# Performance work log

Measured on AMD Instinct MI355X. Metric: run time of the kernel, lower is better.

Reference implementation:

```python
import jax, jax.numpy as jnp
import numpy as np

B, M, V, D = 2048, 2, 25, 64      # batch, max_body, joints, input channels
C1, C2, K, U = 128, 256, 3, 256   # gcn hidden, gcn out, A kernel size, lstm units
NJ, NB = M * V * U, M * U         # joint / body state widths
SD = NJ + NB + U                  # full state dim = 13568


def _hs(z):
    # keras hard_sigmoid
    return jnp.clip(0.2 * z + 0.5, 0.0, 1.0)


def _lstm_step(z, c):
    i = _hs(z[..., :U])
    f = _hs(z[..., U:2 * U])
    g = jnp.tanh(z[..., 2 * U:3 * U])
    o = _hs(z[..., 3 * U:])
    c2 = f * c + i * g
    return o * jnp.tanh(c2), c2


def _forget_bias(shape_prefix):
    z = jnp.zeros(shape_prefix + (U,), jnp.float32)
    return jnp.concatenate([z, jnp.ones_like(z), z, z], axis=-1)


def setup_inputs() -> dict:
    key = jax.random.key(0)
    ks = jax.random.split(key, 16)
    f = lambda i, shape, s: jax.random.normal(ks[i], shape, jnp.float32) * s
    x = f(0, (B, M * V * D), 1.0)
    h0 = f(1, (B, SD), 0.1)
    c0 = f(2, (B, SD), 0.1)
    A = jax.random.uniform(ks[3], (K, V, V), jnp.float32)
    A = A / jnp.sum(A, axis=-1, keepdims=True)  # row-normalized adjacency stack
    edge_importance = jnp.ones((2, K, V, V), jnp.float32)
    return dict(
        x=x, h0=h0, c0=c0, A=A, edge_importance=edge_importance,
        wg0=f(4, (D, C1 * K), 0.05), bg0=jnp.zeros((C1 * K,), jnp.float32),
        wg1=f(5, (C1, C2 * K), 0.05), bg1=jnp.zeros((C2 * K,), jnp.float32),
        wr1=f(6, (C1, C2), 0.05), br1=jnp.zeros((C2,), jnp.float32),
        kernel=f(7, (C2, 4 * U), 0.02),
        kernel_body=f(8, (V * C2, 4 * U), 0.01),
        kernel_whole=f(9, (M * V * C2, 4 * U), 0.005),
        rk=f(10, (U, 4 * U), 0.02),
        rk_body=f(11, (U, 4 * U), 0.02),
        rk_whole=f(12, (U, 4 * U), 0.02),
        bias=_forget_bias((M, V)),
        bias_body=_forget_bias((M,)),
        bias_whole=_forget_bias((1,)),
    )


def reference(x, h0, c0, A, edge_importance, wg0, bg0, wg1, bg1, wr1, br1,
              kernel, kernel_body, kernel_whole, rk, rk_body, rk_whole,
              bias, bias_body, bias_whole):
    N = B * M
    xg = x.reshape(N, V, D)
    # --- GCN layer 0: 1x1 conv -> split K -> edge-weighted adjacency einsum ---
    y = (xg @ wg0 + bg0).reshape(N, V, K, C1)
    y = jnp.einsum('nvkc,kvw->nwc', y, edge_importance[0] * A)
    y = jax.nn.relu(y)
    # --- GCN layer 1 (channels change -> residual 1x1 conv) ---
    res = y @ wr1 + br1
    z = (y @ wg1 + bg1).reshape(N, V, K, C2)
    z = jnp.einsum('nvkc,kvw->nwc', z, edge_importance[1] * A) + res
    feat = jax.nn.relu(z).reshape(B, M, V, C2)
    # --- unpack multi-scale state ---
    h_j = h0[:, :NJ].reshape(B, M, V, U)
    c_j = c0[:, :NJ].reshape(B, M, V, U)
    h_b = h0[:, NJ:NJ + NB].reshape(B, M, U)
    c_b = c0[:, NJ:NJ + NB].reshape(B, M, U)
    h_w = h0[:, NJ + NB:]
    c_w = c0[:, NJ + NB:]
    # --- joint-scale gates ---
    zj = jnp.einsum('bmvc,cu->bmvu', feat, kernel) + h_j @ rk + bias
    h_j2, c_j2 = _lstm_step(zj, c_j)
    # --- body-scale gates ---
    zb = feat.reshape(B, M, V * C2) @ kernel_body + h_b @ rk_body + bias_body
    h_b2, c_b2 = _lstm_step(zb, c_b)
    # --- whole-scale gates ---
    zw = feat.reshape(B, M * V * C2) @ kernel_whole + h_w @ rk_whole + bias_whole[0]
    h_w2, c_w2 = _lstm_step(zw, c_w)
    h_new = jnp.concatenate([h_j2.reshape(B, NJ), h_b2.reshape(B, NB), h_w2], axis=-1)
    return h_new
```

## Files before the change

### kernel.cpp

```cpp
#include <hip/hip_runtime.h>
#include <hip/hip_bf16.h>
#include <math.h>

constexpr int Bn = 2048, Mm = 2, Vv = 25, Dd = 64;
constexpr int C1 = 128, C2 = 256, Kk = 3, Uu = 256;
constexpr int NJ = Mm*Vv*Uu;
constexpr int NBd = Mm*Uu;
constexpr int SD = NJ+NBd+Uu;
constexpr int Nn = Bn*Mm;
constexpr int N3 = Nn*Vv;
constexpr int NCH = 2;
constexpr int NnC = Nn/NCH;
constexpr int RCn = NnC*Vv;

typedef __bf16 v8bf __attribute__((ext_vector_type(8)));
typedef float f32x16 __attribute__((ext_vector_type(16)));

__device__ __forceinline__ float hsig(float z){ return fminf(fmaxf(0.2f*z+0.5f,0.f),1.f); }
__device__ __forceinline__ float ftanh(float x){
  float e = __expf(2.f*x);
  return 1.f - 2.f*__frcp_rn(e+1.f);
}
__device__ __forceinline__ unsigned short f2bs(float x){
  __hip_bfloat16 h = __float2bfloat16(x);
  unsigned short s; __builtin_memcpy(&s, &h, 2); return s;
}
__device__ __forceinline__ float bs2f(unsigned short s){
  unsigned u = ((unsigned)s)<<16; float f; __builtin_memcpy(&f,&u,4); return f;
}

#if defined(__has_builtin)
#if __has_builtin(__builtin_amdgcn_global_load_lds)
#define HAS_ALD 1
#endif
#endif
#ifndef HAS_ALD
#define HAS_ALD 0
#endif
__device__ __forceinline__ void stage16(unsigned short* dst_base, int lane, const void* src){
#if HAS_ALD
  __builtin_amdgcn_global_load_lds(
      (const __attribute__((address_space(1))) unsigned int*)src,
      (__attribute__((address_space(3))) unsigned int*)dst_base, 16, 0, 0);
#else
  *(uint4*)(dst_base + lane*8) = *(const uint4*)src;
#endif
}

template<int SW, typename TI>
__global__ __launch_bounds__(SW*3) void kMix(
    const TI* __restrict__ src, const float* __restrict__ Amat,
    const float* __restrict__ ei, int eoff, unsigned short* __restrict__ dst)
{
  __shared__ float xs[Vv*SW];
  __shared__ float as[Kk*Vv*Vv];
  const int n = blockIdx.x, t = threadIdx.x;
  const TI* srow = src + (size_t)n*(Vv*SW);
  for(int i=t;i<Vv*SW;i+=SW*3){
    if constexpr (sizeof(TI)==2) xs[i]=bs2f((unsigned short)srow[i]);
    else xs[i]=srow[i];
  }
  for(int i=t;i<Kk*Vv*Vv;i+=SW*3) as[i]=ei[eoff+i]*Amat[i];
  __syncthreads();
  const int k = t/SW, d = t%SW;
  float acc[Vv];
  #pragma unroll
  for(int w=0;w<Vv;++w) acc[w]=0.f;
  for(int v=0;v<Vv;++v){
    float xv = xs[v*SW+d];
    const float* ap = &as[k*625 + v*25];
    #pragma unroll
    for(int w=0;w<Vv;++w) acc[w] += ap[w]*xv;
  }
  unsigned short* drow = dst + (size_t)n*(Vv*3*SW);
  for(int w=0;w<Vv;++w) drow[w*(3*SW) + t] = f2bs(acc[w]);
}

template<int MODE>
__device__ __forceinline__ size_t hoffOf(int row){
  if constexpr (MODE==0){ int b=row/50, j=row-b*50; return (size_t)b*SD + j*256; }
  else if constexpr (MODE==1){ int b=row>>1, m=row&1; return (size_t)b*SD + NJ + m*256; }
  else return (size_t)row*SD + NJ + NBd;
}

template<int MODE>
__global__ __launch_bounds__(256) void kConvW(
    const float* __restrict__ Wm, const float* __restrict__ Wr,
    unsigned short* __restrict__ out, int total)
{
  int i = blockIdx.x*256 + threadIdx.x;
  if(i>=total) return;
  int e = i&7, ln = (i>>3)&63, l31 = ln&31, l5 = ln>>5;
  float v;
  if constexpr (MODE<=2){
    constexpr int KF = (MODE==0)?256:(MODE==1)?6400:12800;
    constexpr int NKT = (KF+256)/32;
    int fb = (i>>9)&15, kt = (i>>13)%NKT, ublk = i/(NKT*8192);
    int kh = fb&1, cg = fb>>1;
    int k = kt*32 + l5*8 + kh*16 + e;
    int g = cg&3, uu = (cg>>2)*32 + l31;
    int col = g*256 + ublk*64 + uu;
    v = (k<KF) ? Wm[(size_t)k*1024+col] : Wr[(size_t)(k-KF)*1024+col];
  } else if constexpr (MODE==3){
    int fb = (i>>9)&15, kt = i>>13;
    int kh = fb&1, cg = fb>>1;
    int k = kt*32 + l5*8 + kh*16 + e;
    int col = cg*32 + l31;
    v = (k<384) ? Wm[(size_t)(k&127)*768 + (k>>7)*256 + col]
                : Wr[(size_t)(k-384)*256 + col];
  } else {
    int fb = (i>>9)&7, kt = i>>12;
    int kh = fb&1, cg = fb>>1;
    int k = kt*32 + l5*8 + kh*16 + e;
    int col = cg*32 + l31;
    v = Wm[(size_t)(k&63)*384 + (k>>6)*128 + col];
  }
  out[i] = f2bs(v);
}

template<int MODE>
__global__ __launch_bounds__(256) void kConvH(
    const float* __restrict__ h0, unsigned short* __restrict__ dst, int total4)
{
  int i = blockIdx.x*256 + threadIdx.x;
  if(i>=total4) return;
  int row = i>>6, k4 = (i&63)*4;
  const float* s = h0 + hoffOf<MODE>(row) + k4;
  float4 f = *(const float4*)s;
  uint2 o;
  o.x = (unsigned)f2bs(f.x) | ((unsigned)f2bs(f.y)<<16);
  o.y = (unsigned)f2bs(f.z) | ((unsigned)f2bs(f.w)<<16);
  *(uint2*)(dst + (size_t)i*4) = o;
}

template<int MODE, int MR>
__global__ __launch_bounds__(256,2) void kLSTMm(
    const unsigned short* __restrict__ featb, const unsigned short* __restrict__ h0b,
    const float* __restrict__ c0, const unsigned short* __restrict__ Wcat,
    const float* __restrict__ bias, float* __restrict__ outp, int KC)
{
  constexpr int KF = (MODE==0)?256:(MODE==1)?6400:12800;
  constexpr int KT = KF+256;
  constexpr int NKT = KT/32;
  constexpr int ROWS = (MODE==0)?N3:(MODE==1)?Nn:Bn;
  constexpr int NRG = MR/64;
  constexpr int NAF = (MR/32)*2;
  __shared__ unsigned short Afr[2][NAF*512];
  __shared__ unsigned short Bfr[2][16*512];
  const int t = threadIdx.x;
  const int bx = blockIdx.x;
  const int r0 = (bx>>2)*MR;
  const int ublk = bx&3;
  const int z = (MODE==0)?0:blockIdx.y;
  const int kBeg = z*KC, kEnd = min(KT, kBeg+KC);
  const int lane = t&63, wid = t>>6;
  const int wr = wid>>1, w2 = wid&1;
  const int l31 = lane&31, l5 = lane>>5;

  f32x16 acc[NRG][4];
  #pragma unroll
  for(int rg=0;rg<NRG;++rg)
    #pragma unroll
    for(int g=0;g<4;++g)
      #pragma unroll
      for(int j=0;j<16;++j) acc[rg][g][j]=0.f;

  auto stageA = [&](unsigned short* dstb, int k0){
    #pragma unroll
    for(int i=0;i<NRG;++i){
      int fi = i*256 + t;
      int row = r0 + (fi>>7)*32 + l31;
      int kc = (lane>>5) + ((fi>>6)&1)*2;
      int kg = k0 + kc*8;
      const unsigned short* src = (kg < KF)
          ? featb + (size_t)row*KF + kg
          : h0b   + (size_t)row*256 + (kg - KF);
      stage16(dstb + (size_t)(i*256 + wid*64)*8, lane, src);
    }
  };
  auto stageB = [&](unsigned short* dstb, int k0){
    const unsigned short* wt = Wcat + ((size_t)ublk*NKT + (k0>>5))*8192;
    #pragma unroll
    for(int i=0;i<4;++i){
      int fi = i*256 + t;
      stage16(dstb + (size_t)(i*256 + wid*64)*8, lane, wt + (size_t)fi*8);
    }
  };

  stageA(Afr[0], kBeg); stageB(Bfr[0], kBeg);
  __syncthreads();
  const int nst = (kEnd-kBeg)>>5;
  for(int s=0; s<nst; ++s){
    const int cur = s&1;
    if(s+1<nst){ stageA(Afr[cur^1], kBeg+(s+1)*32); stageB(Bfr[cur^1], kBeg+(s+1)*32); }
    #pragma unroll
    for(int kh=0; kh<2; ++kh){
      v8bf a[NRG];
      #pragma unroll
      for(int rg=0;rg<NRG;++rg)
        a[rg] = *(const v8bf*)&Afr[cur][((wr*NRG+rg)*2+kh)*512 + lane*8];
      #pragma unroll
      for(int g=0; g<4; ++g){
        v8bf b = *(const v8bf*)&Bfr[cur][((w2*4+g)*2+kh)*512 + lane*8];
        #pragma unroll
        for(int rg=0;rg<NRG;++rg)
          acc[rg][g] = __builtin_amdgcn_mfma_f32_32x32x16_bf16(a[rg], b, acc[rg][g], 0, 0, 0);
      }
    }
    __syncthreads();
  }

  const int u = ublk*64 + w2*32 + l31;
  if constexpr (MODE==0){
    #pragma unroll
    for(int rg=0;rg<NRG;++rg){
      #pragma unroll
      for(int reg=0; reg<16; ++reg){
        int row = r0 + (wr*NRG+rg)*32 + (reg&3) + 8*(reg>>2) + 4*l5;
        int b = row/50, j = row - b*50;
        size_t hoff = (size_t)b*SD + j*256;
        int boff = j*1024;
        float zi = acc[rg][0][reg] + bias[boff + u];
        float zf = acc[rg][1][reg] + bias[boff + 256 + u];
        float zg = acc[rg][2][reg] + bias[boff + 512 + u];
        float zo = acc[rg][3][reg] + bias[boff + 768 + u];
        float iv=hsig(zi), fv=hsig(zf), gv=ftanh(zg), ov=hsig(zo);
        float cc = c0[hoff+u];
        float c2 = fv*cc + iv*gv;
        outp[hoff+u] = ov*ftanh(c2);
      }
    }
  } else {
    #pragma unroll
    for(int rg=0;rg<NRG;++rg){
      #pragma unroll
      for(int reg=0; reg<16; ++reg){
        int row = r0 + (wr*NRG+rg)*32 + (reg&3) + 8*(reg>>2) + 4*l5;
        float* base = outp + ((size_t)z*ROWS + row)*1024 + u;
        base[0]   = acc[rg][0][reg];
        base[256] = acc[rg][1][reg];
        base[512] = acc[rg][2][reg];
        base[768] = acc[rg][3][reg];
      }
    }
  }
}

__global__ __launch_bounds__(256,2) void kGC2(
    const unsigned short* __restrict__ ycat, const unsigned short* __restrict__ yb,
    const unsigned short* __restrict__ Wc2, const float* __restrict__ bg1,
    const float* __restrict__ br1, const float* __restrict__ Amat,
    const float* __restrict__ ei, unsigned short* __restrict__ featb)
{
  __shared__ unsigned short Afr[2][4*512];
  __shared__ unsigned short Bfr[2][16*512];
  __shared__ float asums[75];
  const int t = threadIdx.x;
  const int r0 = blockIdx.x*64;
  if(t<75){
    int k=t/25, w=t%25; float s=0.f;
    for(int v=0;v<25;++v) s += ei[1875 + k*625+v*25+w]*Amat[k*625+v*25+w];
    asums[t]=s;
  }
  const int lane = t&63, wid = t>>6;
  const int wr = wid>>1, w2 = wid&1;
  const int l31 = lane&31, l5 = lane>>5;
  f32x16 acc[4];
  #pragma unroll
  for(int g=0;g<4;++g)
    #pragma unroll
    for(int j=0;j<16;++j) acc[g][j]=0.f;

  auto stageA = [&](unsigned short* dst, int k0){
    int fi = t;
    int row = r0 + (fi>>7)*32 + l31;
    int kc = (lane>>5) + ((fi>>6)&1)*2;
    int kg = k0 + kc*8;
    const unsigned short* src = (kg<384) ? ycat + (size_t)row*384 + kg
                                         : yb   + (size_t)row*128 + (kg-384);
    stage16(dst + (size_t)(wid*64)*8, lane, src);
  };
  auto stageB = [&](unsigned short* dst, int k0){
    const unsigned short* wt = Wc2 + (size_t)(k0>>5)*8192;
    #pragma unroll
    for(int i=0;i<4;++i){
      int fi = i*256 + t;
      stage16(dst + (size_t)(i*256 + wid*64)*8, lane, wt + (size_t)fi*8);
    }
  };

  stageA(Afr[0],0); stageB(Bfr[0],0);
  __syncthreads();
  for(int s=0; s<16; ++s){
    const int cur = s&1;
    if(s+1<16){ stageA(Afr[cur^1],(s+1)*32); stageB(Bfr[cur^1],(s+1)*32); }
    #pragma unroll
    for(int kh=0; kh<2; ++kh){
      v8bf a = *(const v8bf*)&Afr[cur][(wr*2+kh)*512 + lane*8];
      #pragma unroll
      for(int g=0; g<4; ++g){
        v8bf b = *(const v8bf*)&Bfr[cur][((w2*4+g)*2+kh)*512 + lane*8];
        acc[g] = __builtin_amdgcn_mfma_f32_32x32x16_bf16(a, b, acc[g], 0, 0, 0);
      }
    }
    __syncthreads();
  }
  #pragma unroll
  for(int reg=0; reg<16; ++reg){
    int row = r0 + wr*32 + (reg&3) + 8*(reg>>2) + 4*l5;
    int w = row % 25;
    float a0w = asums[w], a1w = asums[25+w], a2w = asums[50+w];
    #pragma unroll
    for(int g=0; g<4; ++g){
      int cc = w2*128 + g*32 + l31;
      float b = br1[cc] + a0w*bg1[cc] + a1w*bg1[256+cc] + a2w*bg1[512+cc];
      featb[(size_t)row*256 + cc] = f2bs(fmaxf(acc[g][reg] + b, 0.f));
    }
  }
}

__global__ __launch_bounds__(256,2) void kGC1(
    const unsigned short* __restrict__ xcat, const unsigned short* __restrict__ Wc1,
    const float* __restrict__ bg0, const float* __restrict__ Amat,
    const float* __restrict__ ei, unsigned short* __restrict__ yb)
{
  __shared__ unsigned short Afr[2][4*512];
  __shared__ unsigned short Bfr[2][8*512];
  __shared__ float asums[75];
  const int t = threadIdx.x;
  const int r0 = blockIdx.x*64;
  if(t<75){
    int k=t/25, w=t%25; float s=0.f;
    for(int v=0;v<25;++v) s += ei[k*625+v*25+w]*Amat[k*625+v*25+w];
    asums[t]=s;
  }
  const int lane = t&63, wid = t>>6;
  const int wr = wid>>1, w2 = wid&1;
  const int l31 = lane&31, l5 = lane>>5;
  f32x16 acc[2];
  #pragma unroll
  for(int g=0;g<2;++g)
    #pragma unroll
    for(int j=0;j<16;++j) acc[g][j]=0.f;

  auto stageA = [&](unsigned short* dst, int k0){
    int fi = t;
    int row = r0 + (fi>>7)*32 + l31;
    int kc = (lane>>5) + ((fi>>6)&1)*2;
    int kg = k0 + kc*8;
    stage16(dst + (size_t)(wid*64)*8, lane, xcat + (size_t)row*192 + kg);
  };
  auto stageB = [&](unsigned short* dst, int k0){
    const unsigned short* wt = Wc1 + (size_t)(k0>>5)*4096;
    #pragma unroll
    for(int i=0;i<2;++i){
      int fi = i*256 + t;
      stage16(dst + (size_t)(i*256 + wid*64)*8, lane, wt + (size_t)fi*8);
    }
  };

  stageA(Afr[0],0); stageB(Bfr[0],0);
  __syncthreads();
  for(int s=0; s<6; ++s){
    const int cur = s&1;
    if(s+1<6){ stageA(Afr[cur^1],(s+1)*32); stageB(Bfr[cur^1],(s+1)*32); }
    #pragma unroll
    for(int kh=0; kh<2; ++kh){
      v8bf a = *(const v8bf*)&Afr[cur][(wr*2+kh)*512 + lane*8];
      #pragma unroll
      for(int g=0; g<2; ++g){
        v8bf b = *(const v8bf*)&Bfr[cur][((w2*2+g)*2+kh)*512 + lane*8];
        acc[g] = __builtin_amdgcn_mfma_f32_32x32x16_bf16(a, b, acc[g], 0, 0, 0);
      }
    }
    __syncthreads();
  }
  #pragma unroll
  for(int reg=0; reg<16; ++reg){
    int row = r0 + wr*32 + (reg&3) + 8*(reg>>2) + 4*l5;
    int w = row % 25;
    float a0w = asums[w], a1w = asums[25+w], a2w = asums[50+w];
    #pragma unroll
    for(int g=0; g<2; ++g){
      int cc = w2*64 + g*32 + l31;
      float b = a0w*bg0[cc] + a1w*bg0[128+cc] + a2w*bg0[256+cc];
      yb[(size_t)row*128 + cc] = f2bs(fmaxf(acc[g][reg] + b, 0.f));
    }
  }
}

template<int MODE>
__global__ __launch_bounds__(256) void kFin(
    const float* __restrict__ part, const float* __restrict__ c0,
    const float* __restrict__ bias, float* __restrict__ out, int S)
{
  constexpr int ROWS = (MODE==1)?Nn:Bn;
  const int row = blockIdx.x, u = threadIdx.x;
  size_t hoff = hoffOf<MODE>(row);
  int boff = (MODE==1)?((row&1)*1024):0;
  float zg4[4] = { bias[boff+u], bias[boff+256+u], bias[boff+512+u], bias[boff+768+u] };
  for(int s=0;s<S;++s){
    const float* p = part + ((size_t)s*ROWS + row)*1024;
    #pragma unroll
    for(int g=0;g<4;++g) zg4[g] += p[g*256+u];
  }
  float iv=hsig(zg4[0]), fv=hsig(zg4[1]), gv=ftanh(zg4[2]), ov=hsig(zg4[3]);
  float cc = c0[hoff+u];
  float c2 = fv*cc + iv*gv;
  out[hoff+u] = ov*ftanh(c2);
}

extern "C" void kernel_launch(void* const* d_in, const int* in_sizes, int n_in,
                              void* d_out, int out_size, void* d_ws, size_t ws_size,
                              hipStream_t stream)
{
  const float* x   = (const float*)d_in[0];
  const float* h0  = (const float*)d_in[1];
  const float* c0  = (const float*)d_in[2];
  const float* A   = (const float*)d_in[3];
  const float* ei  = (const float*)d_in[4];
  const float* wg0 = (const float*)d_in[5];
  const float* bg0 = (const float*)d_in[6];
  const float* wg1 = (const float*)d_in[7];
  const float* bg1 = (const float*)d_in[8];
  const float* wr1 = (const float*)d_in[9];
  const float* br1 = (const float*)d_in[10];
  const float* kern  = (const float*)d_in[11];
  const float* kernB = (const float*)d_in[12];
  const float* kernW = (const float*)d_in[13];
  const float* rk    = (const float*)d_in[14];
  const float* rkB   = (const float*)d_in[15];
  const float* rkW   = (const float*)d_in[16];
  const float* bias  = (const float*)d_in[17];
  const float* biasB = (const float*)d_in[18];
  const float* biasW = (const float*)d_in[19];
  float* out = (float*)d_out;
  char* wsb  = (char*)d_ws;

  unsigned short* featb = (unsigned short*)wsb;
  unsigned short* WbJ = (unsigned short*)(wsb + 52428800);
  unsigned short* WbB = WbJ + 524288;
  unsigned short* WbW = WbB + 6815744;
  unsigned short* Wc2 = WbW + 13369344;
  unsigned short* Wc1 = Wc2 + 131072;
  char* dyn = wsb + 94158848;
  unsigned short* ycat = (unsigned short*)dyn;
  unsigned short* xcat = ycat;
  unsigned short* yb   = (unsigned short*)(dyn + 39321600);
  unsigned short* h0bJ = (unsigned short*)dyn;
  float* part = (float*)dyn;
  unsigned short* hB = (unsigned short*)(wsb + 146587648);
  unsigned short* hW = hB + 1048576;

  kConvW<0><<<(524288+255)/256,   256, 0, stream>>>(kern,  rk,  WbJ, 524288);
  kConvW<1><<<(6815744+255)/256,  256, 0, stream>>>(kernB, rkB, WbB, 6815744);
  kConvW<2><<<(13369344+255)/256, 256, 0, stream>>>(kernW, rkW, WbW, 13369344);
  kConvW<3><<<(131072+255)/256,   256, 0, stream>>>(wg1, wr1, Wc2, 131072);
  kConvW<4><<<(24576+255)/256,    256, 0, stream>>>(wg0, nullptr, Wc1, 24576);
  kConvH<1><<<(262144+255)/256, 256, 0, stream>>>(h0, hB, 262144);
  kConvH<2><<<(131072+255)/256, 256, 0, stream>>>(h0, hW, 131072);

  for(int c=0;c<NCH;++c){
    const float* xc = x + (size_t)c*NnC*(Vv*Dd);
    kMix<64,float>          <<<NnC, 192, 0, stream>>>(xc, A, ei, 0, xcat);
    kGC1<<<RCn/64, 256, 0, stream>>>(xcat, Wc1, bg0, A, ei, yb);
    kMix<128,unsigned short><<<NnC, 384, 0, stream>>>(yb, A, ei, 1875, ycat);
    kGC2<<<RCn/64, 256, 0, stream>>>(ycat, yb, Wc2, bg1, br1, A, ei,
                                     featb + (size_t)c*RCn*256);
  }
  kConvH<0><<<(6553600+255)/256, 256, 0, stream>>>(h0, h0bJ, 6553600);
  kLSTMm<0,64><<<(N3/64)*4, 256, 0, stream>>>(featb, h0bJ, c0, WbJ, bias, out, 512);
  kLSTMm<1,128><<<dim3((Nn/128)*4,3), 256, 0, stream>>>(featb, hB, nullptr, WbB, nullptr, part, 2240);
  kFin<1><<<Nn, 256, 0, stream>>>(part, c0, biasB, out, 3);
  kLSTMm<2,128><<<dim3((Bn/128)*4,6), 256, 0, stream>>>(featb, hW, nullptr, WbW, nullptr, part, 2176);
  kFin<2><<<Bn, 256, 0, stream>>>(part, c0, biasW, out, 6);
}
```

Baseline: 746.3 us.

## Load GEMM B fragments directly into registers and shrink LSTM row tiles

```diff
diff --git a/kernel.cpp b/kernel.cpp
--- a/kernel.cpp
+++ b/kernel.cpp
@@ -133,7 +133,7 @@
   *(uint2*)(dst + (size_t)i*4) = o;
 }
 
-template<int MODE, int MR>
+template<int MODE>
 __global__ __launch_bounds__(256,2) void kLSTMm(
     const unsigned short* __restrict__ featb, const unsigned short* __restrict__ h0b,
     const float* __restrict__ c0, const unsigned short* __restrict__ Wcat,
@@ -143,13 +143,10 @@
   constexpr int KT = KF+256;
   constexpr int NKT = KT/32;
   constexpr int ROWS = (MODE==0)?N3:(MODE==1)?Nn:Bn;
-  constexpr int NRG = MR/64;
-  constexpr int NAF = (MR/32)*2;
-  __shared__ unsigned short Afr[2][NAF*512];
-  __shared__ unsigned short Bfr[2][16*512];
+  __shared__ unsigned short Afr[2][4*512];
   const int t = threadIdx.x;
   const int bx = blockIdx.x;
-  const int r0 = (bx>>2)*MR;
+  const int r0 = (bx>>2)*64;
   const int ublk = bx&3;
   const int z = (MODE==0)?0:blockIdx.y;
   const int kBeg = z*KC, kEnd = min(KT, kBeg+KC);
@@ -157,91 +154,78 @@
   const int wr = wid>>1, w2 = wid&1;
   const int l31 = lane&31, l5 = lane>>5;
 
-  f32x16 acc[NRG][4];
-  #pragma unroll
-  for(int rg=0;rg<NRG;++rg)
-    #pragma unroll
-    for(int g=0;g<4;++g)
-      #pragma unroll
-      for(int j=0;j<16;++j) acc[rg][g][j]=0.f;
+  f32x16 acc[4];
+  #pragma unroll
+  for(int g=0;g<4;++g)
+    #pragma unroll
+    for(int j=0;j<16;++j) acc[g][j]=0.f;
 
   auto stageA = [&](unsigned short* dstb, int k0){
-    #pragma unroll
-    for(int i=0;i<NRG;++i){
-      int fi = i*256 + t;
-      int row = r0 + (fi>>7)*32 + l31;
-      int kc = (lane>>5) + ((fi>>6)&1)*2;
-      int kg = k0 + kc*8;
-      const unsigned short* src = (kg < KF)
-          ? featb + (size_t)row*KF + kg
-          : h0b   + (size_t)row*256 + (kg - KF);
-      stage16(dstb + (size_t)(i*256 + wid*64)*8, lane, src);
-    }
-  };
-  auto stageB = [&](unsigned short* dstb, int k0){
-    const unsigned short* wt = Wcat + ((size_t)ublk*NKT + (k0>>5))*8192;
-    #pragma unroll
-    for(int i=0;i<4;++i){
-      int fi = i*256 + t;
-      stage16(dstb + (size_t)(i*256 + wid*64)*8, lane, wt + (size_t)fi*8);
-    }
-  };
-
-  stageA(Afr[0], kBeg); stageB(Bfr[0], kBeg);
+    int row = r0 + wr*32 + l31;
+    int kg = k0 + (w2*2 + l5)*8;
+    const unsigned short* src = (kg < KF)
+        ? featb + (size_t)row*KF + kg
+        : h0b   + (size_t)row*256 + (kg - KF);
+    stage16(dstb + (size_t)(wid*64)*8, lane, src);
+  };
+  auto loadB = [&](v8bf (&b)[8], int k0){
+    const unsigned short* wt = Wcat + ((size_t)ublk*NKT + (k0>>5))*8192 + (size_t)lane*8;
+    #pragma unroll
+    for(int g=0; g<4; ++g)
+      #pragma unroll
+      for(int kh=0; kh<2; ++kh)
+        b[g*2+kh] = *(const v8bf*)(wt + ((w2*4+g)*2+kh)*512);
+  };
+  auto mstep = [&](const v8bf (&b)[8], const unsigned short* Ab){
+    #pragma unroll
+    for(int kh=0; kh<2; ++kh){
+      v8bf a = *(const v8bf*)&Ab[(wr*2+kh)*512 + lane*8];
+      #pragma unroll
+      for(int g=0; g<4; ++g)
+        acc[g] = __builtin_amdgcn_mfma_f32_32x32x16_bf16(a, b[g*2+kh], acc[g], 0, 0, 0);
+    }
+  };
+
+  v8bf bA[8], bB[8];
+  stageA(Afr[0], kBeg); loadB(bA, kBeg);
   __syncthreads();
   const int nst = (kEnd-kBeg)>>5;
-  for(int s=0; s<nst; ++s){
-    const int cur = s&1;
-    if(s+1<nst){ stageA(Afr[cur^1], kBeg+(s+1)*32); stageB(Bfr[cur^1], kBeg+(s+1)*32); }
-    #pragma unroll
-    for(int kh=0; kh<2; ++kh){
-      v8bf a[NRG];
-      #pragma unroll
-      for(int rg=0;rg<NRG;++rg)
-        a[rg] = *(const v8bf*)&Afr[cur][((wr*NRG+rg)*2+kh)*512 + lane*8];
-      #pragma unroll
-      for(int g=0; g<4; ++g){
-        v8bf b = *(const v8bf*)&Bfr[cur][((w2*4+g)*2+kh)*512 + lane*8];
-        #pragma unroll
-        for(int rg=0;rg<NRG;++rg)
-          acc[rg][g] = __builtin_amdgcn_mfma_f32_32x32x16_bf16(a[rg], b, acc[rg][g], 0, 0, 0);
-      }
-    }
+  for(int s=0; s<nst; s+=2){
+    int k0 = kBeg + s*32;
+    stageA(Afr[1], k0+32); loadB(bB, k0+32);
+    mstep(bA, Afr[0]);
+    __syncthreads();
+    if(s+2<nst){ stageA(Afr[0], k0+64); loadB(bA, k0+64); }
+    mstep(bB, Afr[1]);
     __syncthreads();
   }
 
   const int u = ublk*64 + w2*32 + l31;
   if constexpr (MODE==0){
     #pragma unroll
-    for(int rg=0;rg<NRG;++rg){
-      #pragma unroll
-      for(int reg=0; reg<16; ++reg){
-        int row = r0 + (wr*NRG+rg)*32 + (reg&3) + 8*(reg>>2) + 4*l5;
-        int b = row/50, j = row - b*50;
-        size_t hoff = (size_t)b*SD + j*256;
-        int boff = j*1024;
-        float zi = acc[rg][0][reg] + bias[boff + u];
-        float zf = acc[rg][1][reg] + bias[boff + 256 + u];
-        float zg = acc[rg][2][reg] + bias[boff + 512 + u];
-        float zo = acc[rg][3][reg] + bias[boff + 768 + u];
-        float iv=hsig(zi), fv=hsig(zf), gv=ftanh(zg), ov=hsig(zo);
-        float cc = c0[hoff+u];
-        float c2 = fv*cc + iv*gv;
-        outp[hoff+u] = ov*ftanh(c2);
-      }
+    for(int reg=0; reg<16; ++reg){
+      int row = r0 + wr*32 + (reg&3) + 8*(reg>>2) + 4*l5;
+      int b = row/50, j = row - b*50;
+      size_t hoff = (size_t)b*SD + j*256;
+      int boff = j*1024;
+      float zi = acc[0][reg] + bias[boff + u];
+      float zf = acc[1][reg] + bias[boff + 256 + u];
+      float zg = acc[2][reg] + bias[boff + 512 + u];
+      float zo = acc[3][reg] + bias[boff + 768 + u];
+      float iv=hsig(zi), fv=hsig(zf), gv=ftanh(zg), ov=hsig(zo);
+      float cc = c0[hoff+u];
+      float c2 = fv*cc + iv*gv;
+      outp[hoff+u] = ov*ftanh(c2);
     }
   } else {
     #pragma unroll
-    for(int rg=0;rg<NRG;++rg){
-      #pragma unroll
-      for(int reg=0; reg<16; ++reg){
-        int row = r0 + (wr*NRG+rg)*32 + (reg&3) + 8*(reg>>2) + 4*l5;
-        float* base = outp + ((size_t)z*ROWS + row)*1024 + u;
-        base[0]   = acc[rg][0][reg];
-        base[256] = acc[rg][1][reg];
-        base[512] = acc[rg][2][reg];
-        base[768] = acc[rg][3][reg];
-      }
+    for(int reg=0; reg<16; ++reg){
+      int row = r0 + wr*32 + (reg&3) + 8*(reg>>2) + 4*l5;
+      float* base = outp + ((size_t)z*ROWS + row)*1024 + u;
+      base[0]   = acc[0][reg];
+      base[256] = acc[1][reg];
+      base[512] = acc[2][reg];
+      base[768] = acc[3][reg];
     }
   }
 }
@@ -253,7 +237,6 @@
     const float* __restrict__ ei, unsigned short* __restrict__ featb)
 {
   __shared__ unsigned short Afr[2][4*512];
-  __shared__ unsigned short Bfr[2][16*512];
   __shared__ float asums[75];
   const int t = threadIdx.x;
   const int r0 = blockIdx.x*64;
@@ -272,37 +255,39 @@
     for(int j=0;j<16;++j) acc[g][j]=0.f;
 
   auto stageA = [&](unsigned short* dst, int k0){
-    int fi = t;
-    int row = r0 + (fi>>7)*32 + l31;
-    int kc = (lane>>5) + ((fi>>6)&1)*2;
-    int kg = k0 + kc*8;
+    int row = r0 + wr*32 + l31;
+    int kg = k0 + (w2*2 + l5)*8;
     const unsigned short* src = (kg<384) ? ycat + (size_t)row*384 + kg
                                          : yb   + (size_t)row*128 + (kg-384);
     stage16(dst + (size_t)(wid*64)*8, lane, src);
   };
-  auto stageB = [&](unsigned short* dst, int k0){
-    const unsigned short* wt = Wc2 + (size_t)(k0>>5)*8192;
-    #pragma unroll
-    for(int i=0;i<4;++i){
-      int fi = i*256 + t;
-      stage16(dst + (size_t)(i*256 + wid*64)*8, lane, wt + (size_t)fi*8);
-    }
-  };
-
-  stageA(Afr[0],0); stageB(Bfr[0],0);
+  auto loadB = [&](v8bf (&b)[8], int k0){
+    const unsigned short* wt = Wc2 + (size_t)(k0>>5)*8192 + (size_t)lane*8;
+    #pragma unroll
+    for(int g=0; g<4; ++g)
+      #pragma unroll
+      for(int kh=0; kh<2; ++kh)
+        b[g*2+kh] = *(const v8bf*)(wt + ((w2*4+g)*2+kh)*512);
+  };
+  auto mstep = [&](const v8bf (&b)[8], const unsigned short* Ab){
+    #pragma unroll
+    for(int kh=0; kh<2; ++kh){
+      v8bf a = *(const v8bf*)&Ab[(wr*2+kh)*512 + lane*8];
+      #pragma unroll
+      for(int g=0; g<4; ++g)
+        acc[g] = __builtin_amdgcn_mfma_f32_32x32x16_bf16(a, b[g*2+kh], acc[g], 0, 0, 0);
+    }
+  };
+
+  v8bf bA[8], bB[8];
+  stageA(Afr[0],0); loadB(bA,0);
   __syncthreads();
-  for(int s=0; s<16; ++s){
-    const int cur = s&1;
-    if(s+1<16){ stageA(Afr[cur^1],(s+1)*32); stageB(Bfr[cur^1],(s+1)*32); }
-    #pragma unroll
-    for(int kh=0; kh<2; ++kh){
-      v8bf a = *(const v8bf*)&Afr[cur][(wr*2+kh)*512 + lane*8];
-      #pragma unroll
-      for(int g=0; g<4; ++g){
-        v8bf b = *(const v8bf*)&Bfr[cur][((w2*4+g)*2+kh)*512 + lane*8];
-        acc[g] = __builtin_amdgcn_mfma_f32_32x32x16_bf16(a, b, acc[g], 0, 0, 0);
-      }
-    }
+  for(int s=0; s<16; s+=2){
+    stageA(Afr[1],(s+1)*32); loadB(bB,(s+1)*32);
+    mstep(bA, Afr[0]);
+    __syncthreads();
+    if(s+2<16){ stageA(Afr[0],(s+2)*32); loadB(bA,(s+2)*32); }
+    mstep(bB, Afr[1]);
     __syncthreads();
   }
   #pragma unroll
@@ -325,7 +310,6 @@
     const float* __restrict__ ei, unsigned short* __restrict__ yb)
 {
   __shared__ unsigned short Afr[2][4*512];
-  __shared__ unsigned short Bfr[2][8*512];
   __shared__ float asums[75];
   const int t = threadIdx.x;
   const int r0 = blockIdx.x*64;
@@ -344,35 +328,37 @@
     for(int j=0;j<16;++j) acc[g][j]=0.f;
 
   auto stageA = [&](unsigned short* dst, int k0){
-    int fi = t;
-    int row = r0 + (fi>>7)*32 + l31;
-    int kc = (lane>>5) + ((fi>>6)&1)*2;
-    int kg = k0 + kc*8;
+    int row = r0 + wr*32 + l31;
+    int kg = k0 + (w2*2 + l5)*8;
     stage16(dst + (size_t)(wid*64)*8, lane, xcat + (size_t)row*192 + kg);
   };
-  auto stageB = [&](unsigned short* dst, int k0){
-    const unsigned short* wt = Wc1 + (size_t)(k0>>5)*4096;
-    #pragma unroll
-    for(int i=0;i<2;++i){
-      int fi = i*256 + t;
-      stage16(dst + (size_t)(i*256 + wid*64)*8, lane, wt + (size_t)fi*8);
-    }
-  };
-
-  stageA(Afr[0],0); stageB(Bfr[0],0);
+  auto loadB = [&](v8bf (&b)[4], int k0){
+    const unsigned short* wt = Wc1 + (size_t)(k0>>5)*4096 + (size_t)lane*8;
+    #pragma unroll
+    for(int g=0; g<2; ++g)
+      #pragma unroll
+      for(int kh=0; kh<2; ++kh)
+        b[g*2+kh] = *(const v8bf*)(wt + ((w2*2+g)*2+kh)*512);
+  };
+  auto mstep = [&](const v8bf (&b)[4], const unsigned short* Ab){
+    #pragma unroll
+    for(int kh=0; kh<2; ++kh){
+      v8bf a = *(const v8bf*)&Ab[(wr*2+kh)*512 + lane*8];
+      #pragma unroll
+      for(int g=0; g<2; ++g)
+        acc[g] = __builtin_amdgcn_mfma_f32_32x32x16_bf16(a, b[g*2+kh], acc[g], 0, 0, 0);
+    }
+  };
+
+  v8bf bA[4], bB[4];
+  stageA(Afr[0],0); loadB(bA,0);
   __syncthreads();
-  for(int s=0; s<6; ++s){
-    const int cur = s&1;
-    if(s+1<6){ stageA(Afr[cur^1],(s+1)*32); stageB(Bfr[cur^1],(s+1)*32); }
-    #pragma unroll
-    for(int kh=0; kh<2; ++kh){
-      v8bf a = *(const v8bf*)&Afr[cur][(wr*2+kh)*512 + lane*8];
-      #pragma unroll
-      for(int g=0; g<2; ++g){
-        v8bf b = *(const v8bf*)&Bfr[cur][((w2*2+g)*2+kh)*512 + lane*8];
-        acc[g] = __builtin_amdgcn_mfma_f32_32x32x16_bf16(a, b, acc[g], 0, 0, 0);
-      }
-    }
+  for(int s=0; s<6; s+=2){
+    stageA(Afr[1],(s+1)*32); loadB(bB,(s+1)*32);
+    mstep(bA, Afr[0]);
+    __syncthreads();
+    if(s+2<6){ stageA(Afr[0],(s+2)*32); loadB(bA,(s+2)*32); }
+    mstep(bB, Afr[1]);
     __syncthreads();
   }
   #pragma unroll
@@ -469,9 +455,9 @@
                                      featb + (size_t)c*RCn*256);
   }
   kConvH<0><<<(6553600+255)/256, 256, 0, stream>>>(h0, h0bJ, 6553600);
-  kLSTMm<0,64><<<(N3/64)*4, 256, 0, stream>>>(featb, h0bJ, c0, WbJ, bias, out, 512);
-  kLSTMm<1,128><<<dim3((Nn/128)*4,3), 256, 0, stream>>>(featb, hB, nullptr, WbB, nullptr, part, 2240);
+  kLSTMm<0><<<(N3/64)*4, 256, 0, stream>>>(featb, h0bJ, c0, WbJ, bias, out, 512);
+  kLSTMm<1><<<dim3((Nn/64)*4,3), 256, 0, stream>>>(featb, hB, nullptr, WbB, nullptr, part, 2240);
   kFin<1><<<Nn, 256, 0, stream>>>(part, c0, biasB, out, 3);
-  kLSTMm<2,128><<<dim3((Bn/128)*4,6), 256, 0, stream>>>(featb, hW, nullptr, WbW, nullptr, part, 2176);
+  kLSTMm<2><<<dim3((Bn/64)*4,6), 256, 0, stream>>>(featb, hW, nullptr, WbW, nullptr, part, 2176);
   kFin<2><<<Bn, 256, 0, stream>>>(part, c0, biasW, out, 6);
 }
```

Result: slower. 795.0 us (+6.5%).

## Use 512-thread blocks with one 32-row tile per wave in MFMA GEMMs

Applied to the files above, without the earlier changes.

```diff
diff --git a/kernel.cpp b/kernel.cpp
--- a/kernel.cpp
+++ b/kernel.cpp
@@ -133,8 +133,8 @@
   *(uint2*)(dst + (size_t)i*4) = o;
 }
 
-template<int MODE, int MR>
-__global__ __launch_bounds__(256,2) void kLSTMm(
+template<int MODE>
+__global__ __launch_bounds__(512,6) void kLSTMm(
     const unsigned short* __restrict__ featb, const unsigned short* __restrict__ h0b,
     const float* __restrict__ c0, const unsigned short* __restrict__ Wcat,
     const float* __restrict__ bias, float* __restrict__ outp, int KC)
@@ -143,13 +143,11 @@
   constexpr int KT = KF+256;
   constexpr int NKT = KT/32;
   constexpr int ROWS = (MODE==0)?N3:(MODE==1)?Nn:Bn;
-  constexpr int NRG = MR/64;
-  constexpr int NAF = (MR/32)*2;
-  __shared__ unsigned short Afr[2][NAF*512];
+  __shared__ unsigned short Afr[2][8*512];
   __shared__ unsigned short Bfr[2][16*512];
   const int t = threadIdx.x;
   const int bx = blockIdx.x;
-  const int r0 = (bx>>2)*MR;
+  const int r0 = (bx>>2)*128;
   const int ublk = bx&3;
   const int z = (MODE==0)?0:blockIdx.y;
   const int kBeg = z*KC, kEnd = min(KT, kBeg+KC);
@@ -157,33 +155,26 @@
   const int wr = wid>>1, w2 = wid&1;
   const int l31 = lane&31, l5 = lane>>5;
 
-  f32x16 acc[NRG][4];
-  #pragma unroll
-  for(int rg=0;rg<NRG;++rg)
-    #pragma unroll
-    for(int g=0;g<4;++g)
-      #pragma unroll
-      for(int j=0;j<16;++j) acc[rg][g][j]=0.f;
+  f32x16 acc[4];
+  #pragma unroll
+  for(int g=0;g<4;++g)
+    #pragma unroll
+    for(int j=0;j<16;++j) acc[g][j]=0.f;
 
   auto stageA = [&](unsigned short* dstb, int k0){
-    #pragma unroll
-    for(int i=0;i<NRG;++i){
-      int fi = i*256 + t;
-      int row = r0 + (fi>>7)*32 + l31;
-      int kc = (lane>>5) + ((fi>>6)&1)*2;
-      int kg = k0 + kc*8;
-      const unsigned short* src = (kg < KF)
-          ? featb + (size_t)row*KF + kg
-          : h0b   + (size_t)row*256 + (kg - KF);
-      stage16(dstb + (size_t)(i*256 + wid*64)*8, lane, src);
-    }
+    int row = r0 + (wid>>1)*32 + l31;
+    int kg = k0 + ((wid&1)*2 + l5)*8;
+    const unsigned short* src = (kg < KF)
+        ? featb + (size_t)row*KF + kg
+        : h0b   + (size_t)row*256 + (kg - KF);
+    stage16(dstb + (size_t)(wid*64)*8, lane, src);
   };
   auto stageB = [&](unsigned short* dstb, int k0){
     const unsigned short* wt = Wcat + ((size_t)ublk*NKT + (k0>>5))*8192;
     #pragma unroll
-    for(int i=0;i<4;++i){
-      int fi = i*256 + t;
-      stage16(dstb + (size_t)(i*256 + wid*64)*8, lane, wt + (size_t)fi*8);
+    for(int i=0;i<2;++i){
+      int off = i*512 + wid*64;
+      stage16(dstb + (size_t)off*8, lane, wt + (size_t)(off + lane)*8);
     }
   };
 
@@ -195,16 +186,11 @@
     if(s+1<nst){ stageA(Afr[cur^1], kBeg+(s+1)*32); stageB(Bfr[cur^1], kBeg+(s+1)*32); }
     #pragma unroll
     for(int kh=0; kh<2; ++kh){
-      v8bf a[NRG];
-      #pragma unroll
-      for(int rg=0;rg<NRG;++rg)
-        a[rg] = *(const v8bf*)&Afr[cur][((wr*NRG+rg)*2+kh)*512 + lane*8];
+      v8bf a = *(const v8bf*)&Afr[cur][((wr*2+kh)*512 + lane*8)];
       #pragma unroll
       for(int g=0; g<4; ++g){
         v8bf b = *(const v8bf*)&Bfr[cur][((w2*4+g)*2+kh)*512 + lane*8];
-        #pragma unroll
-        for(int rg=0;rg<NRG;++rg)
-          acc[rg][g] = __builtin_amdgcn_mfma_f32_32x32x16_bf16(a[rg], b, acc[rg][g], 0, 0, 0);
+        acc[g] = __builtin_amdgcn_mfma_f32_32x32x16_bf16(a, b, acc[g], 0, 0, 0);
       }
     }
     __syncthreads();
@@ -213,50 +199,44 @@
   const int u = ublk*64 + w2*32 + l31;
   if constexpr (MODE==0){
     #pragma unroll
-    for(int rg=0;rg<NRG;++rg){
-      #pragma unroll
-      for(int reg=0; reg<16; ++reg){
-        int row = r0 + (wr*NRG+rg)*32 + (reg&3) + 8*(reg>>2) + 4*l5;
-        int b = row/50, j = row - b*50;
-        size_t hoff = (size_t)b*SD + j*256;
-        int boff = j*1024;
-        float zi = acc[rg][0][reg] + bias[boff + u];
-        float zf = acc[rg][1][reg] + bias[boff + 256 + u];
-        float zg = acc[rg][2][reg] + bias[boff + 512 + u];
-        float zo = acc[rg][3][reg] + bias[boff + 768 + u];
-        float iv=hsig(zi), fv=hsig(zf), gv=ftanh(zg), ov=hsig(zo);
-        float cc = c0[hoff+u];
-        float c2 = fv*cc + iv*gv;
-        outp[hoff+u] = ov*ftanh(c2);
-      }
+    for(int reg=0; reg<16; ++reg){
+      int row = r0 + wr*32 + (reg&3) + 8*(reg>>2) + 4*l5;
+      int b = row/50, j = row - b*50;
+      size_t hoff = (size_t)b*SD + j*256;
+      int boff = j*1024;
+      float zi = acc[0][reg] + bias[boff + u];
+      float zf = acc[1][reg] + bias[boff + 256 + u];
+      float zg = acc[2][reg] + bias[boff + 512 + u];
+      float zo = acc[3][reg] + bias[boff + 768 + u];
+      float iv=hsig(zi), fv=hsig(zf), gv=ftanh(zg), ov=hsig(zo);
+      float cc = c0[hoff+u];
+      float c2 = fv*cc + iv*gv;
+      outp[hoff+u] = ov*ftanh(c2);
     }
   } else {
     #pragma unroll
-    for(int rg=0;rg<NRG;++rg){
-      #pragma unroll
-      for(int reg=0; reg<16; ++reg){
-        int row = r0 + (wr*NRG+rg)*32 + (reg&3) + 8*(reg>>2) + 4*l5;
-        float* base = outp + ((size_t)z*ROWS + row)*1024 + u;
-        base[0]   = acc[rg][0][reg];
-        base[256] = acc[rg][1][reg];
-        base[512] = acc[rg][2][reg];
-        base[768] = acc[rg][3][reg];
-      }
-    }
-  }
-}
-
-__global__ __launch_bounds__(256,2) void kGC2(
+    for(int reg=0; reg<16; ++reg){
+      int row = r0 + wr*32 + (reg&3) + 8*(reg>>2) + 4*l5;
+      float* base = outp + ((size_t)z*ROWS + row)*1024 + u;
+      base[0]   = acc[0][reg];
+      base[256] = acc[1][reg];
+      base[512] = acc[2][reg];
+      base[768] = acc[3][reg];
+    }
+  }
+}
+
+__global__ __launch_bounds__(512,6) void kGC2(
     const unsigned short* __restrict__ ycat, const unsigned short* __restrict__ yb,
     const unsigned short* __restrict__ Wc2, const float* __restrict__ bg1,
     const float* __restrict__ br1, const float* __restrict__ Amat,
     const float* __restrict__ ei, unsigned short* __restrict__ featb)
 {
-  __shared__ unsigned short Afr[2][4*512];
+  __shared__ unsigned short Afr[2][8*512];
   __shared__ unsigned short Bfr[2][16*512];
   __shared__ float asums[75];
   const int t = threadIdx.x;
-  const int r0 = blockIdx.x*64;
+  const int r0 = blockIdx.x*128;
   if(t<75){
     int k=t/25, w=t%25; float s=0.f;
     for(int v=0;v<25;++v) s += ei[1875 + k*625+v*25+w]*Amat[k*625+v*25+w];
@@ -272,10 +252,8 @@
     for(int j=0;j<16;++j) acc[g][j]=0.f;
 
   auto stageA = [&](unsigned short* dst, int k0){
-    int fi = t;
-    int row = r0 + (fi>>7)*32 + l31;
-    int kc = (lane>>5) + ((fi>>6)&1)*2;
-    int kg = k0 + kc*8;
+    int row = r0 + (wid>>1)*32 + l31;
+    int kg = k0 + ((wid&1)*2 + l5)*8;
     const unsigned short* src = (kg<384) ? ycat + (size_t)row*384 + kg
                                          : yb   + (size_t)row*128 + (kg-384);
     stage16(dst + (size_t)(wid*64)*8, lane, src);
@@ -283,9 +261,9 @@
   auto stageB = [&](unsigned short* dst, int k0){
     const unsigned short* wt = Wc2 + (size_t)(k0>>5)*8192;
     #pragma unroll
-    for(int i=0;i<4;++i){
-      int fi = i*256 + t;
-      stage16(dst + (size_t)(i*256 + wid*64)*8, lane, wt + (size_t)fi*8);
+    for(int i=0;i<2;++i){
+      int off = i*512 + wid*64;
+      stage16(dst + (size_t)off*8, lane, wt + (size_t)(off + lane)*8);
     }
   };
 
@@ -319,16 +297,16 @@
   }
 }
 
-__global__ __launch_bounds__(256,2) void kGC1(
+__global__ __launch_bounds__(512,6) void kGC1(
     const unsigned short* __restrict__ xcat, const unsigned short* __restrict__ Wc1,
     const float* __restrict__ bg0, const float* __restrict__ Amat,
     const float* __restrict__ ei, unsigned short* __restrict__ yb)
 {
-  __shared__ unsigned short Afr[2][4*512];
+  __shared__ unsigned short Afr[2][8*512];
   __shared__ unsigned short Bfr[2][8*512];
   __shared__ float asums[75];
   const int t = threadIdx.x;
-  const int r0 = blockIdx.x*64;
+  const int r0 = blockIdx.x*128;
   if(t<75){
     int k=t/25, w=t%25; float s=0.f;
     for(int v=0;v<25;++v) s += ei[k*625+v*25+w]*Amat[k*625+v*25+w];
@@ -344,19 +322,14 @@
     for(int j=0;j<16;++j) acc[g][j]=0.f;
 
   auto stageA = [&](unsigned short* dst, int k0){
-    int fi = t;
-    int row = r0 + (fi>>7)*32 + l31;
-    int kc = (lane>>5) + ((fi>>6)&1)*2;
-    int kg = k0 + kc*8;
+    int row = r0 + (wid>>1)*32 + l31;
+    int kg = k0 + ((wid&1)*2 + l5)*8;
     stage16(dst + (size_t)(wid*64)*8, lane, xcat + (size_t)row*192 + kg);
   };
   auto stageB = [&](unsigned short* dst, int k0){
     const unsigned short* wt = Wc1 + (size_t)(k0>>5)*4096;
-    #pragma unroll
-    for(int i=0;i<2;++i){
-      int fi = i*256 + t;
-      stage16(dst + (size_t)(i*256 + wid*64)*8, lane, wt + (size_t)fi*8);
-    }
+    int off = wid*64;
+    stage16(dst + (size_t)off*8, lane, wt + (size_t)(off + lane)*8);
   };
 
   stageA(Afr[0],0); stageB(Bfr[0],0);
@@ -463,15 +436,15 @@
   for(int c=0;c<NCH;++c){
     const float* xc = x + (size_t)c*NnC*(Vv*Dd);
     kMix<64,float>          <<<NnC, 192, 0, stream>>>(xc, A, ei, 0, xcat);
-    kGC1<<<RCn/64, 256, 0, stream>>>(xcat, Wc1, bg0, A, ei, yb);
+    kGC1<<<RCn/128, 512, 0, stream>>>(xcat, Wc1, bg0, A, ei, yb);
     kMix<128,unsigned short><<<NnC, 384, 0, stream>>>(yb, A, ei, 1875, ycat);
-    kGC2<<<RCn/64, 256, 0, stream>>>(ycat, yb, Wc2, bg1, br1, A, ei,
-                                     featb + (size_t)c*RCn*256);
+    kGC2<<<RCn/128, 512, 0, stream>>>(ycat, yb, Wc2, bg1, br1, A, ei,
+                                      featb + (size_t)c*RCn*256);
   }
   kConvH<0><<<(6553600+255)/256, 256, 0, stream>>>(h0, h0bJ, 6553600);
-  kLSTMm<0,64><<<(N3/64)*4, 256, 0, stream>>>(featb, h0bJ, c0, WbJ, bias, out, 512);
-  kLSTMm<1,128><<<dim3((Nn/128)*4,3), 256, 0, stream>>>(featb, hB, nullptr, WbB, nullptr, part, 2240);
+  kLSTMm<0><<<(N3/128)*4, 512, 0, stream>>>(featb, h0bJ, c0, WbJ, bias, out, 512);
+  kLSTMm<1><<<dim3((Nn/128)*4,3), 512, 0, stream>>>(featb, hB, nullptr, WbB, nullptr, part, 2240);
   kFin<1><<<Nn, 256, 0, stream>>>(part, c0, biasB, out, 3);
-  kLSTMm<2,128><<<dim3((Bn/128)*4,6), 256, 0, stream>>>(featb, hW, nullptr, WbW, nullptr, part, 2176);
+  kLSTMm<2><<<dim3((Bn/128)*4,6), 512, 0, stream>>>(featb, hW, nullptr, WbW, nullptr, part, 2176);
   kFin<2><<<Bn, 256, 0, stream>>>(part, c0, biasW, out, 6);
 }
```

Result: slower. 2.498 ms (+234.7%).
